# Optimization experiments

Measured on AMD Instinct MI355X. Metric: run time of the kernel, lower is better.

## Reference

```python
import jax, jax.numpy as jnp
import numpy as np

B, N, DIM = 16, 4096, 256
EXP = 4
COV_EPS = 1e-08


def setup_inputs() -> dict:
    key = jax.random.key(0)
    ks = jax.random.split(key, 9)
    s = 1.0 / np.sqrt(DIM)
    sh = 1.0 / np.sqrt(DIM * EXP)
    return {
        "x": jax.random.normal(ks[0], (B, N, DIM), dtype=jnp.float32),
        # IsoFFN: Linear(dim, 4*dim) -> GELU -> Linear(4*dim, dim) + residual (dropout inactive at eval)
        "W1": jax.random.uniform(ks[1], (DIM, DIM * EXP), minval=-s, maxval=s, dtype=jnp.float32),
        "b1": jnp.zeros((DIM * EXP,), jnp.float32),
        "W2": jax.random.uniform(ks[2], (DIM * EXP, DIM), minval=-sh, maxval=sh, dtype=jnp.float32),
        "b2": jnp.zeros((DIM,), jnp.float32),
        # eigenvalue head: Linear(dim, 3) + Softplus
        "Wval": jax.random.uniform(ks[3], (DIM, 3), minval=-s, maxval=s, dtype=jnp.float32),
        "bval": jnp.zeros((3,), jnp.float32),
        # eigenvector head: Linear(dim, 9)
        "Wvec": jax.random.uniform(ks[4], (DIM, 9), minval=-s, maxval=s, dtype=jnp.float32),
        "bvec": jnp.zeros((9,), jnp.float32),
    }


def reference(x, W1, b1, W2, b2, Wval, bval, Wvec, bvec):
    b, n, c = x.shape
    # IsoFFN (eval mode: dropout = identity), residual connection
    h = x + jax.nn.gelu(x @ W1 + b1) @ W2 + b2
    # eigenvalue head -> positive eigenvalues -> diagonal [B*N, 3, 3]
    eigvals = jax.nn.softplus(h @ Wval + bval).reshape(b * n, 3)
    L = jnp.zeros((b * n, 3, 3), h.dtype).at[:, jnp.arange(3), jnp.arange(3)].set(eigvals)
    # eigenvector head -> batched tiny QR to orthonormalize
    V = (h @ Wvec + bvec).reshape(b * n, 3, 3)
    Q, _ = jnp.linalg.qr(V)  # batched 3x3 QR
    # cov = Q L Q^T
    cov = jnp.einsum('bij,bjk,blk->bil', Q, L, Q).reshape(b, n, 3, 3)
    cov = (cov + jnp.swapaxes(cov, -2, -1)) * 0.5
    cov = cov + COV_EPS * jnp.eye(3, dtype=cov.dtype)
    return cov
```

## Files before the change

kernel.cpp:

```cpp
#include <hip/hip_runtime.h>
#include <cstdint>
#include <cstddef>

#define TOKENS   65536
#define KDIM     256
#define HIDDEN   1024
#define BM       128
#define HC       64
#define NCHUNK   16
#define NTHREADS 512
#define NBLOCKS  (TOKENS / BM)

using f16x8 = __attribute__((ext_vector_type(8))) _Float16;
using f16x4 = __attribute__((ext_vector_type(4))) _Float16;
using f32x4 = __attribute__((ext_vector_type(4))) float;

__device__ __align__(16) _Float16 g_W1h[NCHUNK * HC * KDIM];
__device__ __align__(16) _Float16 g_W1l[NCHUNK * HC * KDIM];
__device__ __align__(16) _Float16 g_W2h[NCHUNK * KDIM * HC];
__device__ __align__(16) _Float16 g_W2l[NCHUNK * KDIM * HC];
__device__ __align__(16) _Float16 g_Whh[16 * KDIM];
__device__ __align__(16) _Float16 g_Whl[16 * KDIM];

__global__ __launch_bounds__(256) void prep_kernel(
    const float* __restrict__ W1, const float* __restrict__ W2,
    const float* __restrict__ Wval, const float* __restrict__ Wvec) {
  const int tid = blockIdx.x * 256 + threadIdx.x;
  if (tid < 32768) {
    const int c = tid >> 11, rem = tid & 2047;
    const int n = rem & 63, g = rem >> 6;
    const uint32_t p = ((uint32_t)((n * 512 + g * 16) ^ ((n & 7) << 4))) >> 1;
    const int base = c * 16384;
    const int hid = c * 64 + n;
#pragma unroll
    for (int j = 0; j < 8; ++j) {
      const float wv = W1[(g * 8 + j) * HIDDEN + hid];
      const _Float16 hi = (_Float16)wv;
      g_W1h[base + p + j] = hi;
      g_W1l[base + p + j] = (_Float16)(wv - (float)hi);
    }
  } else if (tid < 65536) {
    const int t = tid - 32768;
    const int c = t >> 11, rem = t & 2047;
    const int n = rem & 255, g = rem >> 8;
    const uint32_t p = ((uint32_t)((n * 128 + g * 16) ^ ((n & 7) << 4))) >> 1;
    const int base = c * 16384;
#pragma unroll
    for (int j = 0; j < 8; ++j) {
      const float wv = W2[(c * 64 + g * 8 + j) * KDIM + n];
      const _Float16 hi = (_Float16)wv;
      g_W2h[base + p + j] = hi;
      g_W2l[base + p + j] = (_Float16)(wv - (float)hi);
    }
  } else if (tid < 65536 + 4096) {
    const int e = tid - 65536;
    const int j16 = e >> 8, k = e & 255;
    float wv = 0.f;
    if (j16 < 3) wv = Wval[k * 3 + j16];
    else if (j16 < 12) wv = Wvec[k * 9 + (j16 - 3)];
    const _Float16 hi = (_Float16)wv;
    g_Whh[e] = hi;
    g_Whl[e] = (_Float16)(wv - (float)hi);
  }
}

__device__ __forceinline__ void stage_wave_32k(const char* gsrc, char* ldst,
                                               int w, int lane) {
#pragma unroll
  for (int i = 0; i < 4; ++i) {
    const int o = w * 4096 + i * 1024;
    __builtin_amdgcn_global_load_lds(
        (__attribute__((address_space(1))) void*)(void*)(gsrc + o + lane * 16),
        (__attribute__((address_space(3))) void*)(ldst + o), 16, 0, 0);
  }
}

__global__ __launch_bounds__(NTHREADS, 2) void fused_kernel(
    const float* __restrict__ x, const float* __restrict__ b1,
    const float* __restrict__ b2, const float* __restrict__ bval,
    const float* __restrict__ bvec, float* __restrict__ out) {
  extern __shared__ char smem[];
  const int tid  = threadIdx.x;
  const int lane = tid & 63;
  const int w    = tid >> 6;
  const int wm   = w >> 1;
  const int wn   = w & 1;
  const int l15  = lane & 15;
  const int lg   = lane >> 4;
  const int64_t R = (int64_t)blockIdx.x * BM;

  {
    const float* xg = x + R * KDIM;
#pragma unroll
    for (int i = 0; i < 16; ++i) {
      const int fidx = tid + NTHREADS * i;
      const int row  = fidx >> 6;
      const int f4   = fidx & 63;
      const float4 v = *(const float4*)(xg + row * KDIM + f4 * 4);
      const _Float16 h0 = (_Float16)v.x, h1 = (_Float16)v.y,
                     h2 = (_Float16)v.z, h3 = (_Float16)v.w;
      f16x4 hv = {h0, h1, h2, h3};
      f16x4 lv = {(_Float16)(v.x - (float)h0), (_Float16)(v.y - (float)h1),
                  (_Float16)(v.z - (float)h2), (_Float16)(v.w - (float)h3)};
      const uint32_t off = (uint32_t)(row * 512) +
                           (((uint32_t)(f4 * 8)) ^ ((row & 7) << 4));
      *(f16x4*)(smem + off)         = hv;
      *(f16x4*)(smem + 65536 + off) = lv;
    }
  }
  __syncthreads();

  f16x8 xah[2][8], xal[2][8];
#pragma unroll
  for (int mt = 0; mt < 2; ++mt) {
    const int row = wm * 32 + mt * 16 + l15;
    const uint32_t rbase = row * 512;
    const uint32_t swz = (row & 7) << 4;
#pragma unroll
    for (int ks = 0; ks < 8; ++ks) {
      const uint32_t off = rbase + (((uint32_t)((ks * 32 + lg * 8) * 2)) ^ swz);
      xah[mt][ks] = *(const f16x8*)(smem + off);
      xal[mt][ks] = *(const f16x8*)(smem + 65536 + off);
    }
  }
  __syncthreads();

  const f32x4 z4 = {0.f, 0.f, 0.f, 0.f};
  f32x4 acc2[2][8];
#pragma unroll
  for (int mt = 0; mt < 2; ++mt)
#pragma unroll
    for (int nt = 0; nt < 8; ++nt) acc2[mt][nt] = z4;

#pragma unroll 1
  for (int hc = 0; hc < NCHUNK; ++hc) {
    {
      const size_t cb = (size_t)hc * 32768;
      stage_wave_32k((const char*)g_W1h + cb, smem,         w, lane);
      stage_wave_32k((const char*)g_W1l + cb, smem + 32768, w, lane);
      stage_wave_32k((const char*)g_W2h + cb, smem + 65536, w, lane);
      stage_wave_32k((const char*)g_W2l + cb, smem + 98304, w, lane);
    }
    __syncthreads();

    f32x4 accG[2][2] = {{z4, z4}, {z4, z4}};
#pragma unroll
    for (int ks = 0; ks < 8; ++ks) {
      f16x8 bh[2], bl[2];
#pragma unroll
      for (int nt = 0; nt < 2; ++nt) {
        const int n = wn * 32 + nt * 16 + l15;
        const uint32_t off = (uint32_t)(n * 512) +
                             (((uint32_t)((ks * 32 + lg * 8) * 2)) ^ ((n & 7) << 4));
        bh[nt] = *(const f16x8*)(smem + off);
        bl[nt] = *(const f16x8*)(smem + 32768 + off);
      }
#pragma unroll
      for (int mt = 0; mt < 2; ++mt)
#pragma unroll
        for (int nt = 0; nt < 2; ++nt) {
          accG[mt][nt] = __builtin_amdgcn_mfma_f32_16x16x32_f16(xah[mt][ks], bh[nt], accG[mt][nt], 0, 0, 0);
          accG[mt][nt] = __builtin_amdgcn_mfma_f32_16x16x32_f16(xah[mt][ks], bl[nt], accG[mt][nt], 0, 0, 0);
          accG[mt][nt] = __builtin_amdgcn_mfma_f32_16x16x32_f16(xal[mt][ks], bh[nt], accG[mt][nt], 0, 0, 0);
        }
    }
    __syncthreads();

#pragma unroll
    for (int nt = 0; nt < 2; ++nt) {
      const float bv = b1[hc * HC + wn * 32 + nt * 16 + l15];
#pragma unroll
      for (int mt = 0; mt < 2; ++mt) {
#pragma unroll
        for (int r = 0; r < 4; ++r) {
          const float v  = accG[mt][nt][r] + bv;
          const float u  = 0.79788456080286535588f * (v + 0.044715f * v * v * v);
          const float e  = __expf(2.f * u);
          const float th = 1.f - 2.f / (e + 1.f);
          const float gv = 0.5f * v * (1.f + th);
          const _Float16 gh = (_Float16)gv;
          const _Float16 gl = (_Float16)(gv - (float)gh);
          const int grow = wm * 32 + mt * 16 + lg * 4 + r;
          const int gcol = wn * 32 + nt * 16 + l15;
          const uint32_t off = (uint32_t)(grow * 128) +
                               (((uint32_t)(gcol * 2)) ^ ((grow & 7) << 4));
          *(_Float16*)(smem + off)         = gh;
          *(_Float16*)(smem + 16384 + off) = gl;
        }
      }
    }
    __syncthreads();

#pragma unroll
    for (int ks2 = 0; ks2 < 2; ++ks2) {
      const uint32_t k2 = (uint32_t)((ks2 * 32 + lg * 8) * 2);
      f16x8 ah[2], al[2];
#pragma unroll
      for (int mt = 0; mt < 2; ++mt) {
        const int row = wm * 32 + mt * 16 + l15;
        const uint32_t off = (uint32_t)(row * 128) + (k2 ^ ((row & 7) << 4));
        ah[mt] = *(const f16x8*)(smem + off);
        al[mt] = *(const f16x8*)(smem + 16384 + off);
      }
#pragma unroll
      for (int nt = 0; nt < 8; ++nt) {
        const int n = wn * 128 + nt * 16 + l15;
        const uint32_t off = (uint32_t)(n * 128) + (k2 ^ ((n & 7) << 4));
        const f16x8 bh = *(const f16x8*)(smem + 65536 + off);
        const f16x8 bl = *(const f16x8*)(smem + 98304 + off);
#pragma unroll
        for (int mt = 0; mt < 2; ++mt) {
          acc2[mt][nt] = __builtin_amdgcn_mfma_f32_16x16x32_f16(ah[mt], bh, acc2[mt][nt], 0, 0, 0);
          acc2[mt][nt] = __builtin_amdgcn_mfma_f32_16x16x32_f16(ah[mt], bl, acc2[mt][nt], 0, 0, 0);
          acc2[mt][nt] = __builtin_amdgcn_mfma_f32_16x16x32_f16(al[mt], bh, acc2[mt][nt], 0, 0, 0);
        }
      }
    }
    __syncthreads();
  }

  {
    const float* xg = x + R * KDIM;
#pragma unroll
    for (int nt = 0; nt < 8; ++nt) {
      const float bv = b2[wn * 128 + nt * 16 + l15];
#pragma unroll
      for (int mt = 0; mt < 2; ++mt) {
#pragma unroll
        for (int r = 0; r < 4; ++r) {
          const int row = wm * 32 + mt * 16 + lg * 4 + r;
          const int col = wn * 128 + nt * 16 + l15;
          const float h = acc2[mt][nt][r] + xg[row * KDIM + col] + bv;
          acc2[mt][nt][r] = h;
          const uint32_t off = (uint32_t)(row * 512) +
                               (((uint32_t)(col * 2)) ^ ((row & 7) << 4));
          *(_Float16*)(smem + off) = (_Float16)h;
        }
      }
    }
  }
  __syncthreads();

  f32x4 hacc = z4;
  const int hrow = wm * 32 + wn * 16 + l15;
  const uint32_t hbase = hrow * 512;
  const uint32_t hswz  = (hrow & 7) << 4;
#pragma unroll
  for (int ks = 0; ks < 8; ++ks) {
    const uint32_t off = hbase + (((uint32_t)((ks * 32 + lg * 8) * 2)) ^ hswz);
    const f16x8 af  = *(const f16x8*)(smem + off);
    const f16x8 bhf = *(const f16x8*)(g_Whh + l15 * 256 + ks * 32 + lg * 8);
    const f16x8 blf = *(const f16x8*)(g_Whl + l15 * 256 + ks * 32 + lg * 8);
    hacc = __builtin_amdgcn_mfma_f32_16x16x32_f16(af, bhf, hacc, 0, 0, 0);
    hacc = __builtin_amdgcn_mfma_f32_16x16x32_f16(af, blf, hacc, 0, 0, 0);
  }
  __syncthreads();

#pragma unroll
  for (int nt = 0; nt < 8; ++nt) {
#pragma unroll
    for (int mt = 0; mt < 2; ++mt) {
#pragma unroll
      for (int r = 0; r < 4; ++r) {
        const int row = wm * 32 + mt * 16 + lg * 4 + r;
        const int col = wn * 128 + nt * 16 + l15;
        const float h = acc2[mt][nt][r];
        const _Float16 hh = (_Float16)h;
        const uint32_t off = (uint32_t)(row * 512) +
                             (((uint32_t)(col * 2)) ^ ((row & 7) << 4));
        *(_Float16*)(smem + off) = (_Float16)(h - (float)hh);
      }
    }
  }
  __syncthreads();

#pragma unroll
  for (int ks = 0; ks < 8; ++ks) {
    const uint32_t off = hbase + (((uint32_t)((ks * 32 + lg * 8) * 2)) ^ hswz);
    const f16x8 af  = *(const f16x8*)(smem + off);
    const f16x8 bhf = *(const f16x8*)(g_Whh + l15 * 256 + ks * 32 + lg * 8);
    hacc = __builtin_amdgcn_mfma_f32_16x16x32_f16(af, bhf, hacc, 0, 0, 0);
  }
  const float hb = (l15 < 3) ? bval[l15] : ((l15 < 12) ? bvec[l15 - 3] : 0.f);
#pragma unroll
  for (int r = 0; r < 4; ++r) hacc[r] += hb;

  float* hstg = (float*)(smem + 65536);
#pragma unroll
  for (int r = 0; r < 4; ++r) {
    const int row = wm * 32 + wn * 16 + lg * 4 + r;
    hstg[row * 16 + l15] = hacc[r];
  }
  if (lane < 16) {
    const int row = wm * 32 + wn * 16 + lane;
    const float* hs = hstg + row * 16;
    float sp[3];
#pragma unroll
    for (int i = 0; i < 3; ++i) {
      const float s = hs[i];
      sp[i] = fmaxf(s, 0.f) + log1pf(__expf(-fabsf(s)));
    }
    const float a0 = hs[3], a1 = hs[6], a2 = hs[9];
    const float b0 = hs[4], bc1 = hs[7], bc2 = hs[10];
    const float na = a0 * a0 + a1 * a1 + a2 * a2;
    const float ia = 1.f / sqrtf(fmaxf(na, 1e-30f));
    const float q00 = a0 * ia, q01 = a1 * ia, q02 = a2 * ia;
    const float d  = q00 * b0 + q01 * bc1 + q02 * bc2;
    const float u0 = b0 - d * q00, u1 = bc1 - d * q01, u2 = bc2 - d * q02;
    const float nu = u0 * u0 + u1 * u1 + u2 * u2;
    const float iu = 1.f / sqrtf(fmaxf(nu, 1e-30f));
    const float q10 = u0 * iu, q11 = u1 * iu, q12 = u2 * iu;
    const float q20 = q01 * q12 - q02 * q11;
    const float q21 = q02 * q10 - q00 * q12;
    const float q22 = q00 * q11 - q01 * q10;
    const float c00 = sp[0]*q00*q00 + sp[1]*q10*q10 + sp[2]*q20*q20 + 1e-8f;
    const float c11 = sp[0]*q01*q01 + sp[1]*q11*q11 + sp[2]*q21*q21 + 1e-8f;
    const float c22 = sp[0]*q02*q02 + sp[1]*q12*q12 + sp[2]*q22*q22 + 1e-8f;
    const float c01 = sp[0]*q00*q01 + sp[1]*q10*q11 + sp[2]*q20*q21;
    const float c02 = sp[0]*q00*q02 + sp[1]*q10*q12 + sp[2]*q20*q22;
    const float c12 = sp[0]*q01*q02 + sp[1]*q11*q12 + sp[2]*q21*q22;
    float* o = out + (size_t)(R + row) * 9;
    o[0] = c00; o[1] = c01; o[2] = c02;
    o[3] = c01; o[4] = c11; o[5] = c12;
    o[6] = c02; o[7] = c12; o[8] = c22;
  }
}

extern "C" void kernel_launch(void* const* d_in, const int* in_sizes, int n_in,
                              void* d_out, int out_size, void* d_ws, size_t ws_size,
                              hipStream_t stream) {
  const float* x    = (const float*)d_in[0];
  const float* W1   = (const float*)d_in[1];
  const float* b1   = (const float*)d_in[2];
  const float* W2   = (const float*)d_in[3];
  const float* b2   = (const float*)d_in[4];
  const float* Wval = (const float*)d_in[5];
  const float* bval = (const float*)d_in[6];
  const float* Wvec = (const float*)d_in[7];
  const float* bvec = (const float*)d_in[8];
  float* out = (float*)d_out;
  (void)in_sizes; (void)n_in; (void)out_size; (void)d_ws; (void)ws_size;

  hipFuncSetAttribute((const void*)fused_kernel,
                      hipFuncAttributeMaxDynamicSharedMemorySize, 131072);

  prep_kernel<<<272, 256, 0, stream>>>(W1, W2, Wval, Wvec);
  fused_kernel<<<NBLOCKS, NTHREADS, 131072, stream>>>(x, b1, b2, bval, bvec, out);
}
```

Before: 293.6 us.

## Double-buffer weight chunks with async prefetch and halve hidden chunk size

Hidden chunk size drops from 64 to 32 so two chunks of W1/W2 hi/lo planes fit in LDS, and the next-but-one chunk is prefetched with global_load_lds while the current one is computed. Full __syncthreads are replaced by explicit vmcnt/lgkmcnt waits plus raw barriers. GELU output is stored as packed hi/lo pairs and unpacked with perm, b1 is cached in LDS, and the three split-precision MFMA products go to separate accumulators. The prep kernel is rewritten to emit vectorised, re-swizzled layouts to match. The goal is to hide weight-load latency behind MFMA work and cut barrier stalls, at the cost of more LDS (still one block per CU) and twice as many loop iterations.

```diff
diff --git a/kernel.cpp b/kernel.cpp
--- a/kernel.cpp
+++ b/kernel.cpp
@@ -6,14 +6,19 @@
 #define KDIM     256
 #define HIDDEN   1024
 #define BM       128
-#define HC       64
-#define NCHUNK   16
+#define HC       32
+#define NCHUNK   32
 #define NTHREADS 512
 #define NBLOCKS  (TOKENS / BM)
+
+#define GOFF  131072
+#define B1OFF 147456
+#define LDS_BYTES 151552
 
 using f16x8 = __attribute__((ext_vector_type(8))) _Float16;
 using f16x4 = __attribute__((ext_vector_type(4))) _Float16;
 using f32x4 = __attribute__((ext_vector_type(4))) float;
+using u32x4 = __attribute__((ext_vector_type(4))) uint32_t;
 
 __device__ __align__(16) _Float16 g_W1h[NCHUNK * HC * KDIM];
 __device__ __align__(16) _Float16 g_W1l[NCHUNK * HC * KDIM];
@@ -27,31 +32,35 @@
     const float* __restrict__ Wval, const float* __restrict__ Wvec) {
   const int tid = blockIdx.x * 256 + threadIdx.x;
   if (tid < 32768) {
-    const int c = tid >> 11, rem = tid & 2047;
-    const int n = rem & 63, g = rem >> 6;
-    const uint32_t p = ((uint32_t)((n * 512 + g * 16) ^ ((n & 7) << 4))) >> 1;
-    const int base = c * 16384;
-    const int hid = c * 64 + n;
+    const int c = tid >> 10, n = (tid >> 5) & 31, gd = tid & 31;
+    const int g = gd ^ (n & 7);
+    const int hid = c * 32 + n;
+    f16x8 hv, lv;
 #pragma unroll
     for (int j = 0; j < 8; ++j) {
       const float wv = W1[(g * 8 + j) * HIDDEN + hid];
       const _Float16 hi = (_Float16)wv;
-      g_W1h[base + p + j] = hi;
-      g_W1l[base + p + j] = (_Float16)(wv - (float)hi);
-    }
+      hv[j] = hi;
+      lv[j] = (_Float16)(wv - (float)hi);
+    }
+    const int dst = c * 8192 + n * 256 + gd * 8;
+    *(f16x8*)(g_W1h + dst) = hv;
+    *(f16x8*)(g_W1l + dst) = lv;
   } else if (tid < 65536) {
     const int t = tid - 32768;
-    const int c = t >> 11, rem = t & 2047;
-    const int n = rem & 255, g = rem >> 8;
-    const uint32_t p = ((uint32_t)((n * 128 + g * 16) ^ ((n & 7) << 4))) >> 1;
-    const int base = c * 16384;
+    const int c = t >> 10, n = (t >> 2) & 255, gd = t & 3;
+    const int g = gd ^ ((n >> 1) & 3);
+    f16x8 hv, lv;
 #pragma unroll
     for (int j = 0; j < 8; ++j) {
-      const float wv = W2[(c * 64 + g * 8 + j) * KDIM + n];
+      const float wv = W2[(c * 32 + g * 8 + j) * KDIM + n];
       const _Float16 hi = (_Float16)wv;
-      g_W2h[base + p + j] = hi;
-      g_W2l[base + p + j] = (_Float16)(wv - (float)hi);
-    }
+      hv[j] = hi;
+      lv[j] = (_Float16)(wv - (float)hi);
+    }
+    const int dst = c * 8192 + n * 32 + gd * 8;
+    *(f16x8*)(g_W2h + dst) = hv;
+    *(f16x8*)(g_W2l + dst) = lv;
   } else if (tid < 65536 + 4096) {
     const int e = tid - 65536;
     const int j16 = e >> 8, k = e & 255;
@@ -64,15 +73,30 @@
   }
 }
 
-__device__ __forceinline__ void stage_wave_32k(const char* gsrc, char* ldst,
-                                               int w, int lane) {
-#pragma unroll
-  for (int i = 0; i < 4; ++i) {
-    const int o = w * 4096 + i * 1024;
+__device__ __forceinline__ void stage_chunk(char* buf, int c, int w, int lane) {
+  const int plane = w >> 1, half = w & 1;
+  const _Float16* g;
+  if      (plane == 0) g = g_W1h;
+  else if (plane == 1) g = g_W1l;
+  else if (plane == 2) g = g_W2h;
+  else                 g = g_W2l;
+  const char* s = (const char*)g + (size_t)c * 16384 + half * 8192 + lane * 16;
+  char* d = buf + plane * 16384 + half * 8192;
+#pragma unroll
+  for (int i = 0; i < 8; ++i) {
     __builtin_amdgcn_global_load_lds(
-        (__attribute__((address_space(1))) void*)(void*)(gsrc + o + lane * 16),
-        (__attribute__((address_space(3))) void*)(ldst + o), 16, 0, 0);
-  }
+        (__attribute__((address_space(1))) void*)(void*)(s + i * 1024),
+        (__attribute__((address_space(3))) void*)(d + i * 1024), 16, 0, 0);
+  }
+}
+
+__device__ __forceinline__ f16x8 unpack_half(const u32x4 a, const u32x4 b, uint32_t sel) {
+  u32x4 r;
+  r[0] = __builtin_amdgcn_perm(a[1], a[0], sel);
+  r[1] = __builtin_amdgcn_perm(a[3], a[2], sel);
+  r[2] = __builtin_amdgcn_perm(b[1], b[0], sel);
+  r[3] = __builtin_amdgcn_perm(b[3], b[2], sel);
+  return __builtin_bit_cast(f16x8, r);
 }
 
 __global__ __launch_bounds__(NTHREADS, 2) void fused_kernel(
@@ -88,6 +112,12 @@
   const int l15  = lane & 15;
   const int lg   = lane >> 4;
   const int64_t R = (int64_t)blockIdx.x * BM;
+
+  {
+    float* b1l = (float*)(smem + B1OFF);
+    b1l[tid]       = b1[tid];
+    b1l[tid + 512] = b1[tid + 512];
+  }
 
   {
     const float* xg = x + R * KDIM;
@@ -123,7 +153,12 @@
       xal[mt][ks] = *(const f16x8*)(smem + 65536 + off);
     }
   }
-  __syncthreads();
+  asm volatile("s_waitcnt lgkmcnt(0)" ::: "memory");
+  __builtin_amdgcn_s_barrier();
+  __builtin_amdgcn_sched_barrier(0);
+
+  stage_chunk(smem,         0, w, lane);
+  stage_chunk(smem + 65536, 1, w, lane);
 
   const f32x4 z4 = {0.f, 0.f, 0.f, 0.f};
   f32x4 acc2[2][8];
@@ -133,81 +168,78 @@
     for (int nt = 0; nt < 8; ++nt) acc2[mt][nt] = z4;
 
 #pragma unroll 1
-  for (int hc = 0; hc < NCHUNK; ++hc) {
+  for (int t = 0; t < NCHUNK; ++t) {
+    char* buf = smem + ((t & 1) ? 65536 : 0);
+    if (t == NCHUNK - 1) { asm volatile("s_waitcnt vmcnt(0)" ::: "memory"); }
+    else                 { asm volatile("s_waitcnt vmcnt(8)" ::: "memory"); }
+    __builtin_amdgcn_s_barrier();
+    __builtin_amdgcn_sched_barrier(0);
+
+    f32x4 accA[2] = {z4, z4}, accB[2] = {z4, z4}, accC[2] = {z4, z4};
     {
-      const size_t cb = (size_t)hc * 32768;
-      stage_wave_32k((const char*)g_W1h + cb, smem,         w, lane);
-      stage_wave_32k((const char*)g_W1l + cb, smem + 32768, w, lane);
-      stage_wave_32k((const char*)g_W2h + cb, smem + 65536, w, lane);
-      stage_wave_32k((const char*)g_W2l + cb, smem + 98304, w, lane);
-    }
-    __syncthreads();
-
-    f32x4 accG[2][2] = {{z4, z4}, {z4, z4}};
-#pragma unroll
-    for (int ks = 0; ks < 8; ++ks) {
-      f16x8 bh[2], bl[2];
-#pragma unroll
-      for (int nt = 0; nt < 2; ++nt) {
-        const int n = wn * 32 + nt * 16 + l15;
-        const uint32_t off = (uint32_t)(n * 512) +
-                             (((uint32_t)((ks * 32 + lg * 8) * 2)) ^ ((n & 7) << 4));
-        bh[nt] = *(const f16x8*)(smem + off);
-        bl[nt] = *(const f16x8*)(smem + 32768 + off);
-      }
-#pragma unroll
-      for (int mt = 0; mt < 2; ++mt)
-#pragma unroll
-        for (int nt = 0; nt < 2; ++nt) {
-          accG[mt][nt] = __builtin_amdgcn_mfma_f32_16x16x32_f16(xah[mt][ks], bh[nt], accG[mt][nt], 0, 0, 0);
-          accG[mt][nt] = __builtin_amdgcn_mfma_f32_16x16x32_f16(xah[mt][ks], bl[nt], accG[mt][nt], 0, 0, 0);
-          accG[mt][nt] = __builtin_amdgcn_mfma_f32_16x16x32_f16(xal[mt][ks], bh[nt], accG[mt][nt], 0, 0, 0);
+      const int n = wn * 16 + l15;
+      const uint32_t nbase = (uint32_t)(n * 512);
+      const uint32_t nswz  = (uint32_t)((n & 7) << 4);
+#pragma unroll
+      for (int ks = 0; ks < 8; ++ks) {
+        const uint32_t off = nbase + (((uint32_t)(ks * 64 + lg * 16)) ^ nswz);
+        const f16x8 bh = *(const f16x8*)(buf + off);
+        const f16x8 bl = *(const f16x8*)(buf + 16384 + off);
+#pragma unroll
+        for (int mt = 0; mt < 2; ++mt) {
+          accA[mt] = __builtin_amdgcn_mfma_f32_16x16x32_f16(xah[mt][ks], bh, accA[mt], 0, 0, 0);
+          accB[mt] = __builtin_amdgcn_mfma_f32_16x16x32_f16(xah[mt][ks], bl, accB[mt], 0, 0, 0);
+          accC[mt] = __builtin_amdgcn_mfma_f32_16x16x32_f16(xal[mt][ks], bh, accC[mt], 0, 0, 0);
         }
-    }
-    __syncthreads();
-
-#pragma unroll
-    for (int nt = 0; nt < 2; ++nt) {
-      const float bv = b1[hc * HC + wn * 32 + nt * 16 + l15];
+      }
+    }
+
+    {
+      const float bv = ((const float*)(smem + B1OFF))[t * 32 + wn * 16 + l15];
+      const int gcol = wn * 16 + l15;
 #pragma unroll
       for (int mt = 0; mt < 2; ++mt) {
 #pragma unroll
         for (int r = 0; r < 4; ++r) {
-          const float v  = accG[mt][nt][r] + bv;
+          const float v  = accA[mt][r] + accB[mt][r] + accC[mt][r] + bv;
           const float u  = 0.79788456080286535588f * (v + 0.044715f * v * v * v);
           const float e  = __expf(2.f * u);
           const float th = 1.f - 2.f / (e + 1.f);
           const float gv = 0.5f * v * (1.f + th);
           const _Float16 gh = (_Float16)gv;
           const _Float16 gl = (_Float16)(gv - (float)gh);
+          const uint32_t pk = (uint32_t)__builtin_bit_cast(unsigned short, gh) |
+                              ((uint32_t)__builtin_bit_cast(unsigned short, gl) << 16);
           const int grow = wm * 32 + mt * 16 + lg * 4 + r;
-          const int gcol = wn * 32 + nt * 16 + l15;
-          const uint32_t off = (uint32_t)(grow * 128) +
-                               (((uint32_t)(gcol * 2)) ^ ((grow & 7) << 4));
-          *(_Float16*)(smem + off)         = gh;
-          *(_Float16*)(smem + 16384 + off) = gl;
+          const uint32_t off = (uint32_t)(GOFF + grow * 128) +
+                               (((uint32_t)(gcol * 4)) ^ ((grow & 7) << 4));
+          *(uint32_t*)(smem + off) = pk;
         }
       }
     }
-    __syncthreads();
-
-#pragma unroll
-    for (int ks2 = 0; ks2 < 2; ++ks2) {
-      const uint32_t k2 = (uint32_t)((ks2 * 32 + lg * 8) * 2);
+    asm volatile("s_waitcnt lgkmcnt(0)" ::: "memory");
+    __builtin_amdgcn_s_barrier();
+    __builtin_amdgcn_sched_barrier(0);
+
+    {
       f16x8 ah[2], al[2];
 #pragma unroll
       for (int mt = 0; mt < 2; ++mt) {
         const int row = wm * 32 + mt * 16 + l15;
-        const uint32_t off = (uint32_t)(row * 128) + (k2 ^ ((row & 7) << 4));
-        ah[mt] = *(const f16x8*)(smem + off);
-        al[mt] = *(const f16x8*)(smem + 16384 + off);
+        const uint32_t sw = (uint32_t)((row & 7) << 4);
+        const uint32_t base = (uint32_t)(GOFF + row * 128);
+        const u32x4 w0 = *(const u32x4*)(smem + base + (((uint32_t)(lg * 32)) ^ sw));
+        const u32x4 w1 = *(const u32x4*)(smem + base + (((uint32_t)(lg * 32 + 16)) ^ sw));
+        ah[mt] = unpack_half(w0, w1, 0x05040100u);
+        al[mt] = unpack_half(w0, w1, 0x07060302u);
       }
 #pragma unroll
       for (int nt = 0; nt < 8; ++nt) {
         const int n = wn * 128 + nt * 16 + l15;
-        const uint32_t off = (uint32_t)(n * 128) + (k2 ^ ((n & 7) << 4));
-        const f16x8 bh = *(const f16x8*)(smem + 65536 + off);
-        const f16x8 bl = *(const f16x8*)(smem + 98304 + off);
+        const uint32_t off = (uint32_t)(n * 64) +
+                             (((uint32_t)(lg * 16)) ^ (((n >> 1) & 3) << 4));
+        const f16x8 bh = *(const f16x8*)(buf + 32768 + off);
+        const f16x8 bl = *(const f16x8*)(buf + 49152 + off);
 #pragma unroll
         for (int mt = 0; mt < 2; ++mt) {
           acc2[mt][nt] = __builtin_amdgcn_mfma_f32_16x16x32_f16(ah[mt], bh, acc2[mt][nt], 0, 0, 0);
@@ -216,7 +248,10 @@
         }
       }
     }
-    __syncthreads();
+    __builtin_amdgcn_sched_barrier(0);
+    __builtin_amdgcn_s_barrier();
+    __builtin_amdgcn_sched_barrier(0);
+    if (t + 2 < NCHUNK) stage_chunk(buf, t + 2, w, lane);
   }
 
   {
@@ -342,8 +377,8 @@
   (void)in_sizes; (void)n_in; (void)out_size; (void)d_ws; (void)ws_size;
 
   hipFuncSetAttribute((const void*)fused_kernel,
-                      hipFuncAttributeMaxDynamicSharedMemorySize, 131072);
+                      hipFuncAttributeMaxDynamicSharedMemorySize, LDS_BYTES);
 
   prep_kernel<<<272, 256, 0, stream>>>(W1, W2, Wval, Wvec);
-  fused_kernel<<<NBLOCKS, NTHREADS, 131072, stream>>>(x, b1, b2, bval, bvec, out);
-}
+  fused_kernel<<<NBLOCKS, NTHREADS, LDS_BYTES, stream>>>(x, b1, b2, bval, bvec, out);
+}
```

Result: faster. 287.6 us (-2.0%).
